# Performance work log

Hardware: AMD Instinct MI355X
Metric: run time of the kernel (lower is better)

Reference implementation:

```python
import jax, jax.numpy as jnp
import numpy as np

B, D = 512, 512
NOBJ, NWRD = 12, 16  # word_feat rows act as 'objects', object_feat rows as 'words' (arg swap in SentiGAT.forward)
N_OW = NOBJ + NWRD
EPS = 1e-12


def _with_self_loops(src, dst, n):
    return (np.concatenate([src, np.arange(n)]), np.concatenate([dst, np.arange(n)]))

_src = np.tile(np.arange(NOBJ), NWRD)                 # arange(n_obj).repeat(n_words) in torch == tile
_dst = np.repeat(np.arange(NWRD), NOBJ) + NOBJ        # repeat_interleave + offset
SRC_OW, DST_OW = map(jnp.asarray, _with_self_loops(_src, _dst, N_OW))

_E5 = np.array([[0,0,0,0,1,1,1,1,2,2,2,2,3,3,3,3,4,4,4,4],
                [1,2,3,4,0,2,3,4,0,1,3,4,0,1,2,4,0,1,2,3]])
SRC5, DST5 = map(jnp.asarray, _with_self_loops(_E5[0], _E5[1], 5))


def gat_conv(x, src, dst, W, a_src, a_dst, bias, concat, num_nodes):
    """PyG GATConv (add_self_loops already in src/dst, negative_slope=0.2, dropout=0)."""
    heads, out_dim = a_src.shape
    h = (x @ W).reshape(num_nodes, heads, out_dim)
    e = jax.nn.leaky_relu((h * a_src).sum(-1)[src] + (h * a_dst).sum(-1)[dst], 0.2)  # [E, heads]
    m = jax.ops.segment_max(e, dst, num_segments=num_nodes)
    p = jnp.exp(e - m[dst])
    alpha = p / jax.ops.segment_sum(p, dst, num_segments=num_nodes)[dst]             # softmax over incoming edges
    out = jax.ops.segment_sum(alpha[:, :, None] * h[src], dst, num_segments=num_nodes)
    out = out.reshape(num_nodes, heads * out_dim) if concat else out.mean(axis=1)
    return out + bias


def _ind_norm(f):
    # add_feature_indicator + F.normalize(p=2, dim=1, eps=1e-12)
    v = (f.sum(axis=1) != 0).astype(f.dtype)[:, None]
    g = jnp.concatenate([f, v], axis=1)
    return g / jnp.maximum(jnp.linalg.norm(g, axis=1, keepdims=True), EPS)


def setup_inputs() -> dict:
    k = jax.random.split(jax.random.key(0), 32)
    r = lambda i, s: jax.random.normal(k[i], s, dtype=jnp.float32)
    sc = 0.05
    return {
        "text_feat": r(0, (B, D)), "image_feat": r(1, (B, D)), "imgtxt_feat": r(2, (B, D)),
        "face_feat": r(3, (B, D)), "word_feat": r(4, (B, NOBJ, D)), "object_feat": r(5, (B, NWRD, D)),
        "ow_W": r(6, (D, 2 * D)) * sc, "ow_asrc": r(7, (2, D)) * sc, "ow_adst": r(8, (2, D)) * sc,
        "ow_b": jnp.zeros((D,), jnp.float32),
        "g1_W": r(9, (D + 1, D)) * sc, "g1_asrc": r(10, (1, D)) * sc, "g1_adst": r(11, (1, D)) * sc,
        "g1_b": jnp.zeros((D,), jnp.float32),
        "g2_W": r(12, (D, D)) * sc, "g2_asrc": r(13, (1, D)) * sc, "g2_adst": r(14, (1, D)) * sc,
        "g2_b": jnp.zeros((D,), jnp.float32),
        "m1_W": r(15, (5 * D, D)) * sc, "m1_b": jnp.zeros((D,), jnp.float32),
        "m2_W": r(16, (D, 3)) * sc, "m2_b": jnp.zeros((3,), jnp.float32),
    }


def reference(text_feat, image_feat, imgtxt_feat, face_feat, word_feat, object_feat,
              ow_W, ow_asrc, ow_adst, ow_b,
              g1_W, g1_asrc, g1_adst, g1_b,
              g2_W, g2_asrc, g2_adst, g2_b,
              m1_W, m1_b, m2_W, m2_b):
    # --- ObjectWordGAT (object_embs=word_feat, word_embs=object_feat per SentiGAT.forward) ---
    def per_sample(obj, wrd):
        x = jnp.concatenate([obj, wrd], axis=0)                       # [N_OW, D]
        h = gat_conv(x, SRC_OW, DST_OW, ow_W, ow_asrc, ow_adst, ow_b, False, N_OW)
        uo, uw = h[:NOBJ], h[NOBJ:]
        attn = jax.nn.softmax(uo @ uw.T, axis=1)                      # [NOBJ, NWRD]
        return (attn @ uw).mean(axis=0)                               # [D]
    aligned = jax.vmap(per_sample)(word_feat, object_feat)            # [B, D]

    feats = [_ind_norm(f) for f in (text_feat, image_feat, imgtxt_feat, face_feat, aligned)]
    x = jnp.stack(feats, axis=1)                                      # [B, 5, D+1]

    # edge_attr (cosine sims) is ignored by GATConv when edge_dim is None
    def graph5(xb):
        h = gat_conv(xb, SRC5, DST5, g1_W, g1_asrc, g1_adst, g1_b, True, 5)
        h = jax.nn.relu(h)
        return gat_conv(h, SRC5, DST5, g2_W, g2_asrc, g2_adst, g2_b, True, 5)
    x = jax.vmap(graph5)(x)                                           # [B, 5, D]

    fused = x.reshape(B, 5 * D)
    hid = jax.nn.relu(fused @ m1_W + m1_b)                            # dropout = identity (eval)
    return hid @ m2_W + m2_b                                          # [B, 3] logits
```

## Files before the change

### kernel.cpp

```cpp
#include <hip/hip_runtime.h>
#include <hip/hip_bf16.h>
#include <math.h>


#define B_SAMP 512

typedef short short8 __attribute__((ext_vector_type(8)));
typedef float floatx4 __attribute__((ext_vector_type(4)));

__device__ __forceinline__ float lrelu02(float x) { return x > 0.f ? x : 0.2f * x; }

__device__ __forceinline__ unsigned short cvt_bf16(float f) {
    union { float f; unsigned int u; } v; v.f = f;
    unsigned int u = v.u;
    return (unsigned short)((u + 0x7FFFu + ((u >> 16) & 1u)) >> 16);
}
__device__ __forceinline__ float bf2f(unsigned short u) {
    union { unsigned int u; float f; } v; v.u = ((unsigned int)u) << 16;
    return v.f;
}

__global__ __launch_bounds__(256) void prep(
    const float* __restrict__ ow_W, const float* __restrict__ ow_asrc,
    const float* __restrict__ ow_adst,
    const float* __restrict__ g1_W, const float* __restrict__ g2_W,
    const float* __restrict__ m1_W,
    float* __restrict__ vg, unsigned short* __restrict__ owWt,
    unsigned short* __restrict__ g1Wt, unsigned short* __restrict__ g2Wt,
    unsigned short* __restrict__ m1Wt)
{
    __shared__ float T[32][33];
    const int tid = threadIdx.x;
    int bid = blockIdx.x;

    if (bid < 128) {
        const int lane = tid & 63;
        const int gw = bid * 4 + (tid >> 6);
        for (int idx = gw; idx < 2048; idx += 512) {
            int t = idx >> 9, k = idx & 511;
            const float* a = (t < 2) ? (ow_asrc + t * 512) : (ow_adst + (t - 2) * 512);
            const float* wr = ow_W + (size_t)k * 1024 + (t & 1) * 512;
            float s = 0.f;
#pragma unroll
            for (int j = 0; j < 8; ++j) s += wr[lane + 64 * j] * a[lane + 64 * j];
            for (int off = 32; off > 0; off >>= 1) s += __shfl_down(s, off, 64);
            if (lane == 0) vg[idx] = s;
        }
        return;
    }
    bid -= 128;
    const float* W; int ldw, K, Kpad, koff, ktiles; float scale; unsigned short* Wt;
    if (bid < 256)        { W = ow_W;       ldw = 1024; K = 512;  Kpad = 1024; koff = 0;   scale = 0.5f; Wt = owWt; ktiles = 16; }
    else if (bid < 512)   { bid -= 256;  W = ow_W + 512; ldw = 1024; K = 512;  Kpad = 1024; koff = 512; scale = 0.5f; Wt = owWt; ktiles = 16; }
    else if (bid < 784)   { bid -= 512;  W = g1_W; ldw = 512; K = 513;  Kpad = 544;  koff = 0; scale = 1.f; Wt = g1Wt; ktiles = 17; }
    else if (bid < 1040)  { bid -= 784;  W = g2_W; ldw = 512; K = 512;  Kpad = 512;  koff = 0; scale = 1.f; Wt = g2Wt; ktiles = 16; }
    else                  { bid -= 1040; W = m1_W; ldw = 512; K = 2560; Kpad = 2560; koff = 0; scale = 1.f; Wt = m1Wt; ktiles = 80; }
    const int k0 = (bid % ktiles) * 32;
    const int n0 = (bid / ktiles) * 32;
    {
        int kr = tid >> 3, nc = (tid & 7) * 4;
        float4 v = make_float4(0.f, 0.f, 0.f, 0.f);
        if (k0 + kr < K) v = *(const float4*)(W + (size_t)(k0 + kr) * ldw + n0 + nc);
        T[nc + 0][kr] = v.x * scale; T[nc + 1][kr] = v.y * scale;
        T[nc + 2][kr] = v.z * scale; T[nc + 3][kr] = v.w * scale;
    }
    __syncthreads();
    {
        int nr = tid >> 3, kc = (tid & 7) * 4;
        ushort4 w;
        w.x = cvt_bf16(T[nr][kc + 0]);
        w.y = cvt_bf16(T[nr][kc + 1]);
        w.z = cvt_bf16(T[nr][kc + 2]);
        w.w = cvt_bf16(T[nr][kc + 3]);
        *(ushort4*)(Wt + (size_t)(n0 + nr) * Kpad + koff + k0 + kc) = w;
    }
}

__global__ __launch_bounds__(256) void ow_pre(
    const float* __restrict__ wf, const float* __restrict__ of,
    const float* __restrict__ vg,
    unsigned short* __restrict__ zcat)
{
    const int b = blockIdx.x;
    __shared__ float Xs[28][512];
    __shared__ float ss[28][2], sd[28][2];
    __shared__ float alpha[16][2][13];

    const int tid = threadIdx.x;
    const int lane = tid & 63;
    const int wid = tid >> 6;

    for (int idx = tid; idx < 28 * 128; idx += 256) {
        int n = idx >> 7, c = (idx & 127) * 4;
        const float* src = (n < 12) ? (wf + ((size_t)b * 12 + n) * 512)
                                    : (of + ((size_t)b * 16 + (n - 12)) * 512);
        *(float4*)&Xs[n][c] = *(const float4*)(src + c);
    }
    __syncthreads();

    for (int p = wid; p < 112; p += 4) {
        int n = p >> 2, t = p & 3;
        const float* vv = vg + t * 512;
        float s = 0.f;
#pragma unroll
        for (int j = 0; j < 8; ++j) s += Xs[n][lane + 64 * j] * vv[lane + 64 * j];
        for (int off = 32; off > 0; off >>= 1) s += __shfl_down(s, off, 64);
        if (lane == 0) { if (t < 2) ss[n][t] = s; else sd[n][t - 2] = s; }
    }
    __syncthreads();

    if (tid < 32) {
        int w = tid >> 1, h = tid & 1;
        float sdv = sd[12 + w][h];
        float e[13], mx = -1e30f;
        for (int j = 0; j < 12; ++j) { e[j] = lrelu02(ss[j][h] + sdv); mx = fmaxf(mx, e[j]); }
        e[12] = lrelu02(ss[12 + w][h] + sdv); mx = fmaxf(mx, e[12]);
        float den = 0.f;
        for (int j = 0; j < 13; ++j) { e[j] = expf(e[j] - mx); den += e[j]; }
        float inv = 1.f / den;
        for (int j = 0; j < 13; ++j) alpha[w][h][j] = e[j] * inv;
    }
    __syncthreads();

    unsigned short* zb = zcat + (size_t)b * 28 * 1024;
    for (int idx = tid; idx < 12 * 1024; idx += 256) {
        int n = idx >> 10, d = idx & 511;
        zb[idx] = cvt_bf16(Xs[n][d]);
    }
    for (int c = tid; c < 1024; c += 256) {
        int h = c >> 9, d = c & 511;
        float xr[12];
#pragma unroll
        for (int j = 0; j < 12; ++j) xr[j] = Xs[j][d];
#pragma unroll 4
        for (int w = 0; w < 16; ++w) {
            float a = alpha[w][h][12] * Xs[12 + w][d];
#pragma unroll
            for (int j = 0; j < 12; ++j) a += alpha[w][h][j] * xr[j];
            zb[(size_t)(12 + w) * 1024 + c] = cvt_bf16(a);
        }
    }
}

template <int BM, int BN, int WGM, int RELU, int SPLITK, int OBF16>
__global__ __launch_bounds__(256) void gemm_v3(
    const unsigned short* __restrict__ A, int lda,
    const unsigned short* __restrict__ Bt, int ldbt,
    void* __restrict__ Cv, int ldc,
    int M, int N, int K,
    const float* __restrict__ bias)
{
    constexpr int WGN = 4 / WGM;
    constexpr int WM = BM / WGM, WN = BN / WGN;
    constexpr int MF = WM / 16, NF = WN / 16;
    constexpr int CA = (BM * 4 + 255) / 256, CB = (BN * 4 + 255) / 256;

    __shared__ unsigned short As[2][BM][40];
    __shared__ unsigned short Bs[2][BN][40];

    const int tid = threadIdx.x;
    const int m0 = blockIdx.x * BM;
    const int n0 = blockIdx.y * BN;
    const int lane = tid & 63;
    const int wid = tid >> 6;
    const int wm = (wid % WGM) * WM;
    const int wn = (wid / WGM) * WN;
    const int fr = lane & 15;
    const int kq = (lane >> 4) * 8;

    const int kchunk = K / SPLITK;
    const int kbeg = (SPLITK > 1) ? blockIdx.z * kchunk : 0;
    const int kend = kbeg + kchunk;
    float* Cf = (float*)Cv;
    unsigned short* Cb = (unsigned short*)Cv;
    if (SPLITK > 1) Cf += (size_t)blockIdx.z * M * ldc;

    short8 ra[CA], rb[CB];
#define LOADAB(K0)                                                                       \
    do {                                                                                 \
        _Pragma("unroll")                                                                \
        for (int c = 0; c < CA; ++c) {                                                   \
            int id = tid + c * 256;                                                      \
            if (BM * 4 % 256 == 0 || id < BM * 4)                                        \
                ra[c] = *(const short8*)(A + (size_t)(m0 + (id >> 2)) * lda + (K0) + (id & 3) * 8); \
        }                                                                                \
        _Pragma("unroll")                                                                \
        for (int c = 0; c < CB; ++c) {                                                   \
            int id = tid + c * 256;                                                      \
            if (BN * 4 % 256 == 0 || id < BN * 4)                                        \
                rb[c] = *(const short8*)(Bt + (size_t)(n0 + (id >> 2)) * ldbt + (K0) + (id & 3) * 8); \
        }                                                                                \
    } while (0)

    LOADAB(kbeg);

    floatx4 acc[MF][NF];
#pragma unroll
    for (int i = 0; i < MF; ++i)
#pragma unroll
        for (int j = 0; j < NF; ++j) acc[i][j] = (floatx4){0.f, 0.f, 0.f, 0.f};

    int t = 0;
    for (int k0 = kbeg; k0 < kend; k0 += 32, t ^= 1) {
#pragma unroll
        for (int c = 0; c < CA; ++c) {
            int id = tid + c * 256;
            if (BM * 4 % 256 == 0 || id < BM * 4)
                *(short8*)&As[t][id >> 2][(id & 3) * 8] = ra[c];
        }
#pragma unroll
        for (int c = 0; c < CB; ++c) {
            int id = tid + c * 256;
            if (BN * 4 % 256 == 0 || id < BN * 4)
                *(short8*)&Bs[t][id >> 2][(id & 3) * 8] = rb[c];
        }
        __syncthreads();
        if (k0 + 32 < kend) LOADAB(k0 + 32);

        short8 af[MF], bw[NF];
#pragma unroll
        for (int i = 0; i < MF; ++i)
            af[i] = *(const short8*)&As[t][wm + i * 16 + fr][kq];
#pragma unroll
        for (int j = 0; j < NF; ++j)
            bw[j] = *(const short8*)&Bs[t][wn + j * 16 + fr][kq];
#pragma unroll
        for (int i = 0; i < MF; ++i)
#pragma unroll
            for (int j = 0; j < NF; ++j)
                acc[i][j] = __builtin_amdgcn_mfma_f32_16x16x32_bf16(
                    af[i], bw[j], acc[i][j], 0, 0, 0);
    }
#undef LOADAB

    const int fq = lane >> 4;
#pragma unroll
    for (int i = 0; i < MF; ++i) {
#pragma unroll
        for (int j = 0; j < NF; ++j) {
#pragma unroll
            for (int q = 0; q < 4; ++q) {
                int row = m0 + wm + i * 16 + fq * 4 + q;
                int col = n0 + wn + j * 16 + fr;
                float v = acc[i][j][q];
                if (SPLITK == 1 && bias) v += bias[col];
                if (RELU) v = fmaxf(v, 0.f);
                if (OBF16) Cb[(size_t)row * ldc + col] = cvt_bf16(v);
                else       Cf[(size_t)row * ldc + col] = v;
            }
        }
    }
}

__global__ __launch_bounds__(256) void attn_x5(
    const unsigned short* __restrict__ hout,
    const float* __restrict__ tf, const float* __restrict__ im,
    const float* __restrict__ it, const float* __restrict__ fa,
    unsigned short* __restrict__ x5)
{
    const int b = blockIdx.x;
    __shared__ float uo[12][520];
    __shared__ float uw[16][520];
    __shared__ float S[12][16];
    __shared__ float w16[16];
    __shared__ float al[512];

    const int tid = threadIdx.x;
    const int lane = tid & 63;
    const int wid = tid >> 6;
    const unsigned short* hb = hout + (size_t)b * 28 * 512;

    for (int idx = tid; idx < 28 * 64; idx += 256) {
        int n = idx >> 6, c = (idx & 63) * 8;
        short8 v = *(const short8*)(hb + (size_t)n * 512 + c);
        float* row = (n < 12) ? &uo[n][c] : &uw[n - 12][c];
#pragma unroll
        for (int j = 0; j < 8; ++j) row[j] = bf2f((unsigned short)v[j]);
    }
    __syncthreads();

    for (int p = wid; p < 192; p += 4) {
        int i = p >> 4, j = p & 15;
        const float* ua = &uo[i][lane * 8];
        const float* uc = &uw[j][lane * 8];
        float s = 0.f;
#pragma unroll
        for (int d = 0; d < 8; ++d) s += ua[d] * uc[d];
        for (int off = 32; off > 0; off >>= 1) s += __shfl_down(s, off, 64);
        if (lane == 0) S[i][j] = s;
    }
    __syncthreads();

    if (tid < 12) {
        float mx = -1e30f;
        for (int j = 0; j < 16; ++j) mx = fmaxf(mx, S[tid][j]);
        float den = 0.f;
        for (int j = 0; j < 16; ++j) { float p = expf(S[tid][j] - mx); S[tid][j] = p; den += p; }
        float inv = 1.f / den;
        for (int j = 0; j < 16; ++j) S[tid][j] *= inv;
    }
    __syncthreads();

    if (tid < 16) {
        float s = 0.f;
        for (int i = 0; i < 12; ++i) s += S[i][tid];
        w16[tid] = s * (1.f / 12.f);
    }
    __syncthreads();

    for (int d = tid; d < 512; d += 256) {
        float s = 0.f;
#pragma unroll
        for (int j = 0; j < 16; ++j) s += w16[j] * uw[j][d];
        al[d] = s;
    }
    __syncthreads();

    for (int f = wid; f < 5; f += 4) {
        const float* src = (f == 0) ? tf : (f == 1) ? im : (f == 2) ? it : (f == 3) ? fa : nullptr;
        float vals[8];
        float sum = 0.f, sq = 0.f;
#pragma unroll
        for (int j = 0; j < 8; ++j) {
            float v = (f < 4) ? src[(size_t)b * 512 + lane + 64 * j] : al[lane + 64 * j];
            vals[j] = v;
            sum += v;
            sq += v * v;
        }
#pragma unroll
        for (int off = 32; off > 0; off >>= 1) {
            sum += __shfl_xor(sum, off, 64);
            sq  += __shfl_xor(sq,  off, 64);
        }
        float v = (sum != 0.f) ? 1.f : 0.f;
        float nrm = fmaxf(sqrtf(sq + v * v), 1e-12f);
        float inv = 1.f / nrm;
        unsigned short* dst = x5 + ((size_t)b * 5 + f) * 544;
#pragma unroll
        for (int j = 0; j < 8; ++j) dst[lane + 64 * j] = cvt_bf16(vals[j] * inv);
        if (lane == 0) dst[512] = cvt_bf16(v * inv);
        else if (lane < 32) dst[512 + lane] = 0;
    }
}

template <int RELU>
__global__ __launch_bounds__(256) void g5_gat(
    const unsigned short* __restrict__ Hg,
    const float* __restrict__ asrc, const float* __restrict__ adst,
    const float* __restrict__ bias, unsigned short* __restrict__ outp)
{
    const int b = blockIdx.x;
    __shared__ float ss[5], sd[5];
    __shared__ float alpha[5][5];

    const int tid = threadIdx.x;
    const int lane = tid & 63;
    const int wave = tid >> 6;
    const unsigned short* Hb = Hg + (size_t)b * 5 * 512;

    for (int p = wave; p < 10; p += 4) {
        int n = p >> 1, ty = p & 1;
        const unsigned short* hv = Hb + n * 512;
        const float* av = ty ? adst : asrc;
        float s = 0.f;
#pragma unroll
        for (int j = 0; j < 8; ++j) s += bf2f(hv[lane + 64 * j]) * av[lane + 64 * j];
        for (int off = 32; off > 0; off >>= 1) s += __shfl_down(s, off, 64);
        if (lane == 0) { if (ty) sd[n] = s; else ss[n] = s; }
    }
    __syncthreads();

    if (tid < 5) {
        int dn = tid;
        float e[5];
        float mx = -1e30f;
        for (int s = 0; s < 5; ++s) {
            e[s] = lrelu02(ss[s] + sd[dn]);
            mx = fmaxf(mx, e[s]);
        }
        float den = 0.f;
        for (int s = 0; s < 5; ++s) { e[s] = expf(e[s] - mx); den += e[s]; }
        float inv = 1.f / den;
        for (int s = 0; s < 5; ++s) alpha[dn][s] = e[s] * inv;
    }
    __syncthreads();

    for (int d = tid; d < 512; d += 256) {
        float h0 = bf2f(Hb[0 * 512 + d]), h1 = bf2f(Hb[1 * 512 + d]), h2 = bf2f(Hb[2 * 512 + d]);
        float h3 = bf2f(Hb[3 * 512 + d]), h4 = bf2f(Hb[4 * 512 + d]);
        float bd = bias[d];
#pragma unroll
        for (int dn = 0; dn < 5; ++dn) {
            float v = alpha[dn][0] * h0 + alpha[dn][1] * h1 + alpha[dn][2] * h2 +
                      alpha[dn][3] * h3 + alpha[dn][4] * h4 + bd;
            if (RELU) v = fmaxf(v, 0.f);
            outp[((size_t)b * 5 + dn) * 512 + d] = cvt_bf16(v);
        }
    }
}

__global__ __launch_bounds__(64) void final2(
    const float* __restrict__ parts, const float* __restrict__ b1,
    const float* __restrict__ w, const float* __restrict__ bvec,
    float* __restrict__ out)
{
    const int b = blockIdx.x;
    const int lane = threadIdx.x;
    float a0 = 0.f, a1 = 0.f, a2 = 0.f;
#pragma unroll
    for (int j = 0; j < 8; ++j) {
        int d = lane + 64 * j;
        size_t o = (size_t)b * 512 + d;
        float x = parts[o] + parts[262144 + o] + parts[524288 + o] + parts[786432 + o] + b1[d];
        x = fmaxf(x, 0.f);
        a0 += x * w[d * 3 + 0];
        a1 += x * w[d * 3 + 1];
        a2 += x * w[d * 3 + 2];
    }
    for (int off = 32; off > 0; off >>= 1) {
        a0 += __shfl_down(a0, off, 64);
        a1 += __shfl_down(a1, off, 64);
        a2 += __shfl_down(a2, off, 64);
    }
    if (lane == 0) {
        out[b * 3 + 0] = a0 + bvec[0];
        out[b * 3 + 1] = a1 + bvec[1];
        out[b * 3 + 2] = a2 + bvec[2];
    }
}

extern "C" void kernel_launch(void* const* d_in, const int* in_sizes, int n_in,
                              void* d_out, int out_size, void* d_ws, size_t ws_size,
                              hipStream_t stream) {
    const float* text   = (const float*)d_in[0];
    const float* image  = (const float*)d_in[1];
    const float* imgtxt = (const float*)d_in[2];
    const float* face   = (const float*)d_in[3];
    const float* word   = (const float*)d_in[4];
    const float* obj    = (const float*)d_in[5];
    const float* ow_W    = (const float*)d_in[6];
    const float* ow_asrc = (const float*)d_in[7];
    const float* ow_adst = (const float*)d_in[8];
    const float* ow_b    = (const float*)d_in[9];
    const float* g1_W    = (const float*)d_in[10];
    const float* g1_asrc = (const float*)d_in[11];
    const float* g1_adst = (const float*)d_in[12];
    const float* g1_b    = (const float*)d_in[13];
    const float* g2_W    = (const float*)d_in[14];
    const float* g2_asrc = (const float*)d_in[15];
    const float* g2_adst = (const float*)d_in[16];
    const float* g2_b    = (const float*)d_in[17];
    const float* m1_W    = (const float*)d_in[18];
    const float* m1_b    = (const float*)d_in[19];
    const float* m2_W    = (const float*)d_in[20];
    const float* m2_b    = (const float*)d_in[21];

    float* ws = (float*)d_ws;
    float* vg = ws;
    float* hidp = ws + 2048;
    unsigned short* owWt = (unsigned short*)(hidp + 1048576);
    unsigned short* g1Wt = owWt + 524288;
    unsigned short* g2Wt = g1Wt + 278528;
    unsigned short* m1Wt = g2Wt + 262144;
    unsigned short* zcat = m1Wt + 1310720;
    unsigned short* houtb = zcat + 14680064;
    unsigned short* x5b  = houtb + 7340032;
    unsigned short* h1b  = x5b + 1392640;
    unsigned short* fsb  = h1b + 1310720;
    unsigned short* hgb  = fsb + 1310720;

    prep<<<2448, 256, 0, stream>>>(ow_W, ow_asrc, ow_adst, g1_W, g2_W, m1_W,
                                   vg, owWt, g1Wt, g2Wt, m1Wt);

    ow_pre<<<B_SAMP, 256, 0, stream>>>(word, obj, vg, zcat);
    gemm_v3<64, 128, 2, 0, 1, 1><<<dim3(224, 4), 256, 0, stream>>>(
        zcat, 1024, owWt, 1024, houtb, 512, 14336, 512, 1024, ow_b);
    attn_x5<<<B_SAMP, 256, 0, stream>>>(houtb, text, image, imgtxt, face, x5b);

    gemm_v3<32, 64, 1, 0, 1, 1><<<dim3(80, 8), 256, 0, stream>>>(
        x5b, 544, g1Wt, 544, hgb, 512, 2560, 512, 544, nullptr);
    g5_gat<1><<<B_SAMP, 256, 0, stream>>>(hgb, g1_asrc, g1_adst, g1_b, h1b);
    gemm_v3<32, 64, 1, 0, 1, 1><<<dim3(80, 8), 256, 0, stream>>>(
        h1b, 512, g2Wt, 512, hgb, 512, 2560, 512, 512, nullptr);
    g5_gat<0><<<B_SAMP, 256, 0, stream>>>(hgb, g2_asrc, g2_adst, g2_b, fsb);

    gemm_v3<32, 64, 1, 0, 4, 0><<<dim3(16, 8, 4), 256, 0, stream>>>(
        fsb, 2560, m1Wt, 2560, hidp, 512, 512, 512, 2560, nullptr);
    final2<<<B_SAMP, 64, 0, stream>>>(hidp, m1_b, m2_W, m2_b, (float*)d_out);
}
```

Baseline: 135.3 us.

## Add direct global-to-LDS GEMM for big ow projection and enlarge tiles

Adds a new 128x128-tile bf16 MFMA GEMM that stages A and B tiles with global_load_lds straight into shared memory, double-buffered, and uses it for the large word/object projection GEMM (14336x512x1024). The smaller GAT and MLP GEMMs move from 32x64 to 64x64 tiles. The aim is to cut VGPR staging and instruction overhead on the dominant GEMM and to raise reuse per block. The cost is fewer blocks (448, and 320 for the GAT GEMMs) and an unpadded LDS layout that can cause bank conflicts on the fragment reads.

```diff
diff --git a/kernel.cpp b/kernel.cpp
--- a/kernel.cpp
+++ b/kernel.cpp
@@ -18,6 +18,11 @@
 __device__ __forceinline__ float bf2f(unsigned short u) {
     union { unsigned int u; float f; } v; v.u = ((unsigned int)u) << 16;
     return v.f;
+}
+__device__ __forceinline__ void gload_lds16(const unsigned short* g, unsigned short* l) {
+    __builtin_amdgcn_global_load_lds(
+        (const __attribute__((address_space(1))) void*)g,
+        (__attribute__((address_space(3))) void*)l, 16, 0, 0);
 }
 
 __global__ __launch_bounds__(256) void prep(
@@ -138,6 +143,85 @@
 #pragma unroll
             for (int j = 0; j < 12; ++j) a += alpha[w][h][j] * xr[j];
             zb[(size_t)(12 + w) * 1024 + c] = cvt_bf16(a);
+        }
+    }
+}
+
+__global__ __launch_bounds__(256) void gemm_glds(
+    const unsigned short* __restrict__ A, int lda,
+    const unsigned short* __restrict__ Bt, int ldbt,
+    unsigned short* __restrict__ C, int ldc,
+    int K, const float* __restrict__ bias)
+{
+    __shared__ unsigned short As[2][128][32];
+    __shared__ unsigned short Bs[2][128][32];
+
+    const int tid = threadIdx.x;
+    const int lane = tid & 63;
+    const int wid = tid >> 6;
+    const int m0 = blockIdx.x * 128;
+    const int n0 = blockIdx.y * 128;
+
+    const int srow = lane >> 2;
+    const int sseg = (lane & 3) * 8;
+    const unsigned short* ga = A + (size_t)(m0 + wid * 32 + srow) * lda + sseg;
+    const unsigned short* gb = Bt + (size_t)(n0 + wid * 32 + srow) * ldbt + sseg;
+    const size_t a16 = (size_t)16 * lda, b16 = (size_t)16 * ldbt;
+
+#define STAGE(t, K0)                                              \
+    do {                                                          \
+        gload_lds16(ga + (K0), &As[t][wid * 32][0]);              \
+        gload_lds16(ga + (K0) + a16, &As[t][wid * 32 + 16][0]);   \
+        gload_lds16(gb + (K0), &Bs[t][wid * 32][0]);              \
+        gload_lds16(gb + (K0) + b16, &Bs[t][wid * 32 + 16][0]);   \
+    } while (0)
+
+    const int wm = (wid & 1) * 64;
+    const int wn = (wid >> 1) * 64;
+    const int fr = lane & 15;
+    const int kq = (lane >> 4) * 8;
+
+    floatx4 acc[4][4];
+#pragma unroll
+    for (int i = 0; i < 4; ++i)
+#pragma unroll
+        for (int j = 0; j < 4; ++j) acc[i][j] = (floatx4){0.f, 0.f, 0.f, 0.f};
+
+    STAGE(0, 0);
+    __syncthreads();
+
+    int t = 0;
+    for (int k0 = 0; k0 < K; k0 += 32, t ^= 1) {
+        if (k0 + 32 < K) STAGE(t ^ 1, k0 + 32);
+
+        short8 af[4], bw[4];
+#pragma unroll
+        for (int i = 0; i < 4; ++i)
+            af[i] = *(const short8*)&As[t][wm + i * 16 + fr][kq];
+#pragma unroll
+        for (int j = 0; j < 4; ++j)
+            bw[j] = *(const short8*)&Bs[t][wn + j * 16 + fr][kq];
+#pragma unroll
+        for (int i = 0; i < 4; ++i)
+#pragma unroll
+            for (int j = 0; j < 4; ++j)
+                acc[i][j] = __builtin_amdgcn_mfma_f32_16x16x32_bf16(
+                    af[i], bw[j], acc[i][j], 0, 0, 0);
+        __syncthreads();
+    }
+#undef STAGE
+
+    const int fq = lane >> 4;
+#pragma unroll
+    for (int i = 0; i < 4; ++i) {
+#pragma unroll
+        for (int j = 0; j < 4; ++j) {
+#pragma unroll
+            for (int q = 0; q < 4; ++q) {
+                int row = m0 + wm + i * 16 + fq * 4 + q;
+                int col = n0 + wn + j * 16 + fr;
+                C[(size_t)row * ldc + col] = cvt_bf16(acc[i][j][q] + bias[col]);
+            }
         }
     }
 }
@@ -473,18 +557,18 @@
                                    vg, owWt, g1Wt, g2Wt, m1Wt);
 
     ow_pre<<<B_SAMP, 256, 0, stream>>>(word, obj, vg, zcat);
-    gemm_v3<64, 128, 2, 0, 1, 1><<<dim3(224, 4), 256, 0, stream>>>(
-        zcat, 1024, owWt, 1024, houtb, 512, 14336, 512, 1024, ow_b);
+    gemm_glds<<<dim3(112, 4), 256, 0, stream>>>(
+        zcat, 1024, owWt, 1024, houtb, 512, 1024, ow_b);
     attn_x5<<<B_SAMP, 256, 0, stream>>>(houtb, text, image, imgtxt, face, x5b);
 
-    gemm_v3<32, 64, 1, 0, 1, 1><<<dim3(80, 8), 256, 0, stream>>>(
+    gemm_v3<64, 64, 2, 0, 1, 1><<<dim3(40, 8), 256, 0, stream>>>(
         x5b, 544, g1Wt, 544, hgb, 512, 2560, 512, 544, nullptr);
     g5_gat<1><<<B_SAMP, 256, 0, stream>>>(hgb, g1_asrc, g1_adst, g1_b, h1b);
-    gemm_v3<32, 64, 1, 0, 1, 1><<<dim3(80, 8), 256, 0, stream>>>(
+    gemm_v3<64, 64, 2, 0, 1, 1><<<dim3(40, 8), 256, 0, stream>>>(
         h1b, 512, g2Wt, 512, hgb, 512, 2560, 512, 512, nullptr);
     g5_gat<0><<<B_SAMP, 256, 0, stream>>>(hgb, g2_asrc, g2_adst, g2_b, fsb);
 
-    gemm_v3<32, 64, 1, 0, 4, 0><<<dim3(16, 8, 4), 256, 0, stream>>>(
+    gemm_v3<64, 64, 2, 0, 4, 0><<<dim3(8, 8, 4), 256, 0, stream>>>(
         fsb, 2560, m1Wt, 2560, hidp, 512, 512, 512, 2560, nullptr);
     final2<<<B_SAMP, 64, 0, stream>>>(hidp, m1_b, m2_W, m2_b, (float*)d_out);
 }
```

Measured after the change: 130.7 us. -3.4%, faster.

## Reassociate object-word GAT attention to avoid projecting all nodes per sample

Applied to the files above, without the earlier changes.

Restructures the object-word GAT branch algebraically. The GEMM that projected all 28 nodes through ow_W is replaced by a precomputed product of the weight halves (WcR times WsR) applied to the object rows, with attention scores formed against aggregated word inputs plus a bias term. Only the softmax-weighted sum per sample is then projected through ow_W. Normalisation moves into a separate build_x5 kernel, the word input is converted from fp32 to bf16 inside the GEMM, and the other GEMM tiles grow to 64x64. This cuts the large 14336-row GEMM and its bf16 staging traffic, at the cost of extra prep work, more launches and different bf16 rounding points.

```diff
diff --git a/kernel.cpp b/kernel.cpp
--- a/kernel.cpp
+++ b/kernel.cpp
@@ -22,20 +22,23 @@
 
 __global__ __launch_bounds__(256) void prep(
     const float* __restrict__ ow_W, const float* __restrict__ ow_asrc,
-    const float* __restrict__ ow_adst,
+    const float* __restrict__ ow_adst, const float* __restrict__ ow_b,
     const float* __restrict__ g1_W, const float* __restrict__ g2_W,
     const float* __restrict__ m1_W,
-    float* __restrict__ vg, unsigned short* __restrict__ owWt,
+    float* __restrict__ vg, float* __restrict__ wb,
+    unsigned short* __restrict__ owWt,
     unsigned short* __restrict__ g1Wt, unsigned short* __restrict__ g2Wt,
-    unsigned short* __restrict__ m1Wt)
+    unsigned short* __restrict__ m1Wt,
+    unsigned short* __restrict__ WcR, unsigned short* __restrict__ WsR)
 {
     __shared__ float T[32][33];
     const int tid = threadIdx.x;
     int bid = blockIdx.x;
+    const int lane = tid & 63;
+    const int wid = tid >> 6;
 
     if (bid < 128) {
-        const int lane = tid & 63;
-        const int gw = bid * 4 + (tid >> 6);
+        const int gw = bid * 4 + wid;
         for (int idx = gw; idx < 2048; idx += 512) {
             int t = idx >> 9, k = idx & 511;
             const float* a = (t < 2) ? (ow_asrc + t * 512) : (ow_adst + (t - 2) * 512);
@@ -48,7 +51,52 @@
         }
         return;
     }
-    bid -= 128;
+    if (bid < 192) {
+        const int gw = (bid - 128) * 4 + wid;
+        for (int a = gw; a < 1024; a += 256) {
+            const float* wr = (a < 512) ? (ow_W + (size_t)a * 1024)
+                                        : (ow_W + (size_t)(a - 512) * 1024 + 512);
+            float s = 0.f;
+#pragma unroll
+            for (int j = 0; j < 8; ++j) s += wr[lane + 64 * j] * ow_b[lane + 64 * j];
+            for (int off = 32; off > 0; off >>= 1) s += __shfl_down(s, off, 64);
+            if (lane == 0) wb[a] = 0.5f * s;
+        }
+        return;
+    }
+    bid -= 192;
+    if (bid >= 2320) {
+        int x = bid - 2320;
+        if (x < 128) {
+            int base = x * 4096;
+#pragma unroll
+            for (int q = 0; q < 4; ++q) {
+                int eidx = base + q * 1024 + tid * 4;
+                int a = eidx >> 9, n = eidx & 511;
+                const float* src = (a < 512) ? (ow_W + (size_t)a * 1024 + n)
+                                             : (ow_W + (size_t)(a - 512) * 1024 + 512 + n);
+                float4 v = *(const float4*)src;
+                ushort4 w;
+                w.x = cvt_bf16(0.5f * v.x); w.y = cvt_bf16(0.5f * v.y);
+                w.z = cvt_bf16(0.5f * v.z); w.w = cvt_bf16(0.5f * v.w);
+                *(ushort4*)(WcR + (size_t)a * 512 + n) = w;
+            }
+        } else {
+            int base = (x - 128) * 4096;
+#pragma unroll
+            for (int q = 0; q < 4; ++q) {
+                int eidx = base + q * 1024 + tid * 4;
+                int d = eidx >> 9, n = eidx & 511;
+                float4 v1 = *(const float4*)(ow_W + (size_t)d * 1024 + n);
+                float4 v2 = *(const float4*)(ow_W + (size_t)d * 1024 + 512 + n);
+                ushort4 w;
+                w.x = cvt_bf16(0.5f * (v1.x + v2.x)); w.y = cvt_bf16(0.5f * (v1.y + v2.y));
+                w.z = cvt_bf16(0.5f * (v1.z + v2.z)); w.w = cvt_bf16(0.5f * (v1.w + v2.w));
+                *(ushort4*)(WsR + (size_t)d * 512 + n) = w;
+            }
+        }
+        return;
+    }
     const float* W; int ldw, K, Kpad, koff, ktiles; float scale; unsigned short* Wt;
     if (bid < 256)        { W = ow_W;       ldw = 1024; K = 512;  Kpad = 1024; koff = 0;   scale = 0.5f; Wt = owWt; ktiles = 16; }
     else if (bid < 512)   { bid -= 256;  W = ow_W + 512; ldw = 1024; K = 512;  Kpad = 1024; koff = 512; scale = 0.5f; Wt = owWt; ktiles = 16; }
@@ -76,10 +124,10 @@
     }
 }
 
-__global__ __launch_bounds__(256) void ow_pre(
+__global__ __launch_bounds__(256) void ow_zw(
     const float* __restrict__ wf, const float* __restrict__ of,
     const float* __restrict__ vg,
-    unsigned short* __restrict__ zcat)
+    unsigned short* __restrict__ zwb)
 {
     const int b = blockIdx.x;
     __shared__ float Xs[28][512];
@@ -122,11 +170,7 @@
     }
     __syncthreads();
 
-    unsigned short* zb = zcat + (size_t)b * 28 * 1024;
-    for (int idx = tid; idx < 12 * 1024; idx += 256) {
-        int n = idx >> 10, d = idx & 511;
-        zb[idx] = cvt_bf16(Xs[n][d]);
-    }
+    unsigned short* zb = zwb + (size_t)b * 16 * 1024;
     for (int c = tid; c < 1024; c += 256) {
         int h = c >> 9, d = c & 511;
         float xr[12];
@@ -137,14 +181,14 @@
             float a = alpha[w][h][12] * Xs[12 + w][d];
 #pragma unroll
             for (int j = 0; j < 12; ++j) a += alpha[w][h][j] * xr[j];
-            zb[(size_t)(12 + w) * 1024 + c] = cvt_bf16(a);
-        }
-    }
-}
-
-template <int BM, int BN, int WGM, int RELU, int SPLITK, int OBF16>
+            zb[(size_t)w * 1024 + c] = cvt_bf16(a);
+        }
+    }
+}
+
+template <int BM, int BN, int WGM, int RELU, int SPLITK, int OBF16, int AF32>
 __global__ __launch_bounds__(256) void gemm_v3(
-    const unsigned short* __restrict__ A, int lda,
+    const void* __restrict__ Av, int lda,
     const unsigned short* __restrict__ Bt, int ldbt,
     void* __restrict__ Cv, int ldc,
     int M, int N, int K,
@@ -153,7 +197,9 @@
     constexpr int WGN = 4 / WGM;
     constexpr int WM = BM / WGM, WN = BN / WGN;
     constexpr int MF = WM / 16, NF = WN / 16;
-    constexpr int CA = (BM * 4 + 255) / 256, CB = (BN * 4 + 255) / 256;
+    constexpr int CAB = (BM * 4 + 255) / 256;
+    constexpr int CAF = (BM * 8 + 255) / 256;
+    constexpr int CB  = (BN * 4 + 255) / 256;
 
     __shared__ unsigned short As[2][BM][40];
     __shared__ unsigned short Bs[2][BN][40];
@@ -175,15 +221,29 @@
     unsigned short* Cb = (unsigned short*)Cv;
     if (SPLITK > 1) Cf += (size_t)blockIdx.z * M * ldc;
 
-    short8 ra[CA], rb[CB];
-#define LOADAB(K0)                                                                       \
+    short8 ra[CAB]; float4 raf[CAF]; short8 rb[CB];
+
+#define LOADA(K0)                                                                        \
     do {                                                                                 \
-        _Pragma("unroll")                                                                \
-        for (int c = 0; c < CA; ++c) {                                                   \
-            int id = tid + c * 256;                                                      \
-            if (BM * 4 % 256 == 0 || id < BM * 4)                                        \
-                ra[c] = *(const short8*)(A + (size_t)(m0 + (id >> 2)) * lda + (K0) + (id & 3) * 8); \
+        if (AF32) {                                                                      \
+            const float* Af = (const float*)Av;                                          \
+            _Pragma("unroll")                                                            \
+            for (int c = 0; c < CAF; ++c) {                                              \
+                int id = tid + c * 256;                                                  \
+                raf[c] = *(const float4*)(Af + (size_t)(m0 + (id >> 3)) * lda + (K0) + (id & 7) * 4); \
+            }                                                                            \
+        } else {                                                                         \
+            const unsigned short* Ab = (const unsigned short*)Av;                        \
+            _Pragma("unroll")                                                            \
+            for (int c = 0; c < CAB; ++c) {                                              \
+                int id = tid + c * 256;                                                  \
+                if (BM * 4 % 256 == 0 || id < BM * 4)                                    \
+                    ra[c] = *(const short8*)(Ab + (size_t)(m0 + (id >> 2)) * lda + (K0) + (id & 3) * 8); \
+            }                                                                            \
         }                                                                                \
+    } while (0)
+#define LOADB(K0)                                                                        \
+    do {                                                                                 \
         _Pragma("unroll")                                                                \
         for (int c = 0; c < CB; ++c) {                                                   \
             int id = tid + c * 256;                                                      \
@@ -192,7 +252,7 @@
         }                                                                                \
     } while (0)
 
-    LOADAB(kbeg);
+    LOADA(kbeg); LOADB(kbeg);
 
     floatx4 acc[MF][NF];
 #pragma unroll
@@ -202,11 +262,22 @@
 
     int t = 0;
     for (int k0 = kbeg; k0 < kend; k0 += 32, t ^= 1) {
-#pragma unroll
-        for (int c = 0; c < CA; ++c) {
-            int id = tid + c * 256;
-            if (BM * 4 % 256 == 0 || id < BM * 4)
-                *(short8*)&As[t][id >> 2][(id & 3) * 8] = ra[c];
+        if (AF32) {
+#pragma unroll
+            for (int c = 0; c < CAF; ++c) {
+                int id = tid + c * 256;
+                ushort4 w;
+                w.x = cvt_bf16(raf[c].x); w.y = cvt_bf16(raf[c].y);
+                w.z = cvt_bf16(raf[c].z); w.w = cvt_bf16(raf[c].w);
+                *(ushort4*)&As[t][id >> 3][(id & 7) * 4] = w;
+            }
+        } else {
+#pragma unroll
+            for (int c = 0; c < CAB; ++c) {
+                int id = tid + c * 256;
+                if (BM * 4 % 256 == 0 || id < BM * 4)
+                    *(short8*)&As[t][id >> 2][(id & 3) * 8] = ra[c];
+            }
         }
 #pragma unroll
         for (int c = 0; c < CB; ++c) {
@@ -215,7 +286,7 @@
                 *(short8*)&Bs[t][id >> 2][(id & 3) * 8] = rb[c];
         }
         __syncthreads();
-        if (k0 + 32 < kend) LOADAB(k0 + 32);
+        if (k0 + 32 < kend) { LOADA(k0 + 32); LOADB(k0 + 32); }
 
         short8 af[MF], bw[NF];
 #pragma unroll
@@ -231,7 +302,8 @@
                 acc[i][j] = __builtin_amdgcn_mfma_f32_16x16x32_bf16(
                     af[i], bw[j], acc[i][j], 0, 0, 0);
     }
-#undef LOADAB
+#undef LOADA
+#undef LOADB
 
     const int fq = lane >> 4;
 #pragma unroll
@@ -252,55 +324,72 @@
     }
 }
 
-__global__ __launch_bounds__(256) void attn_x5(
-    const unsigned short* __restrict__ hout,
-    const float* __restrict__ tf, const float* __restrict__ im,
-    const float* __restrict__ it, const float* __restrict__ fa,
-    unsigned short* __restrict__ x5)
+__global__ __launch_bounds__(256) void ow_attn(
+    const unsigned short* __restrict__ Xq,
+    const unsigned short* __restrict__ zwb,
+    const float* __restrict__ wb,
+    unsigned short* __restrict__ Y)
 {
     const int b = blockIdx.x;
-    __shared__ float uo[12][520];
-    __shared__ float uw[16][520];
+    __shared__ unsigned short xqs[12][1024];
+    __shared__ unsigned short zws[16][1024];
     __shared__ float S[12][16];
+    __shared__ float dj[16];
     __shared__ float w16[16];
-    __shared__ float al[512];
 
     const int tid = threadIdx.x;
     const int lane = tid & 63;
     const int wid = tid >> 6;
-    const unsigned short* hb = hout + (size_t)b * 28 * 512;
-
-    for (int idx = tid; idx < 28 * 64; idx += 256) {
-        int n = idx >> 6, c = (idx & 63) * 8;
-        short8 v = *(const short8*)(hb + (size_t)n * 512 + c);
-        float* row = (n < 12) ? &uo[n][c] : &uw[n - 12][c];
-#pragma unroll
-        for (int j = 0; j < 8; ++j) row[j] = bf2f((unsigned short)v[j]);
-    }
-    __syncthreads();
-
-    for (int p = wid; p < 192; p += 4) {
-        int i = p >> 4, j = p & 15;
-        const float* ua = &uo[i][lane * 8];
-        const float* uc = &uw[j][lane * 8];
+
+    for (int idx = tid; idx < 12 * 128; idx += 256) {
+        int r = idx >> 7, c = (idx & 127) * 8;
+        *(short8*)&xqs[r][c] = *(const short8*)(Xq + ((size_t)b * 12 + r) * 1024 + c);
+    }
+    for (int idx = tid; idx < 16 * 128; idx += 256) {
+        int r = idx >> 7, c = (idx & 127) * 8;
+        *(short8*)&zws[r][c] = *(const short8*)(zwb + ((size_t)b * 16 + r) * 1024 + c);
+    }
+    __syncthreads();
+
+    for (int p = wid; p < 208; p += 4) {
         float s = 0.f;
-#pragma unroll
-        for (int d = 0; d < 8; ++d) s += ua[d] * uc[d];
+        if (p < 192) {
+            int i = p >> 4, j = p & 15;
+#pragma unroll
+            for (int e = 0; e < 8; ++e) {
+                int a = e * 128 + lane * 2;
+                unsigned int xv = *(const unsigned int*)&xqs[i][a];
+                unsigned int zv = *(const unsigned int*)&zws[j][a];
+                s += bf2f((unsigned short)(xv & 0xffff)) * bf2f((unsigned short)(zv & 0xffff))
+                   + bf2f((unsigned short)(xv >> 16))    * bf2f((unsigned short)(zv >> 16));
+            }
+        } else {
+            int j = p - 192;
+#pragma unroll
+            for (int e = 0; e < 8; ++e) {
+                int a = e * 128 + lane * 2;
+                unsigned int zv = *(const unsigned int*)&zws[j][a];
+                s += bf2f((unsigned short)(zv & 0xffff)) * wb[a]
+                   + bf2f((unsigned short)(zv >> 16))    * wb[a + 1];
+            }
+        }
         for (int off = 32; off > 0; off >>= 1) s += __shfl_down(s, off, 64);
-        if (lane == 0) S[i][j] = s;
+        if (lane == 0) { if (p < 192) S[p >> 4][p & 15] = s; else dj[p - 192] = s; }
     }
     __syncthreads();
 
     if (tid < 12) {
         float mx = -1e30f;
-        for (int j = 0; j < 16; ++j) mx = fmaxf(mx, S[tid][j]);
+        for (int j = 0; j < 16; ++j) mx = fmaxf(mx, S[tid][j] + dj[j]);
         float den = 0.f;
-        for (int j = 0; j < 16; ++j) { float p = expf(S[tid][j] - mx); S[tid][j] = p; den += p; }
+        for (int j = 0; j < 16; ++j) {
+            float p = expf(S[tid][j] + dj[j] - mx);
+            S[tid][j] = p; den += p;
+        }
         float inv = 1.f / den;
         for (int j = 0; j < 16; ++j) S[tid][j] *= inv;
     }
     __syncthreads();
-
     if (tid < 16) {
         float s = 0.f;
         for (int i = 0; i < 12; ++i) s += S[i][tid];
@@ -308,39 +397,57 @@
     }
     __syncthreads();
 
-    for (int d = tid; d < 512; d += 256) {
-        float s = 0.f;
-#pragma unroll
-        for (int j = 0; j < 16; ++j) s += w16[j] * uw[j][d];
-        al[d] = s;
-    }
-    __syncthreads();
-
-    for (int f = wid; f < 5; f += 4) {
-        const float* src = (f == 0) ? tf : (f == 1) ? im : (f == 2) ? it : (f == 3) ? fa : nullptr;
-        float vals[8];
-        float sum = 0.f, sq = 0.f;
-#pragma unroll
-        for (int j = 0; j < 8; ++j) {
-            float v = (f < 4) ? src[(size_t)b * 512 + lane + 64 * j] : al[lane + 64 * j];
-            vals[j] = v;
-            sum += v;
-            sq += v * v;
-        }
-#pragma unroll
-        for (int off = 32; off > 0; off >>= 1) {
-            sum += __shfl_xor(sum, off, 64);
-            sq  += __shfl_xor(sq,  off, 64);
-        }
-        float v = (sum != 0.f) ? 1.f : 0.f;
-        float nrm = fmaxf(sqrtf(sq + v * v), 1e-12f);
-        float inv = 1.f / nrm;
-        unsigned short* dst = x5 + ((size_t)b * 5 + f) * 544;
-#pragma unroll
-        for (int j = 0; j < 8; ++j) dst[lane + 64 * j] = cvt_bf16(vals[j] * inv);
-        if (lane == 0) dst[512] = cvt_bf16(v * inv);
-        else if (lane < 32) dst[512 + lane] = 0;
-    }
+    {
+        int a0 = tid * 4;
+        float acc0 = 0.f, acc1 = 0.f, acc2 = 0.f, acc3 = 0.f;
+#pragma unroll
+        for (int j = 0; j < 16; ++j) {
+            float wj = w16[j];
+            ushort4 z4 = *(const ushort4*)&zws[j][a0];
+            acc0 += wj * bf2f(z4.x); acc1 += wj * bf2f(z4.y);
+            acc2 += wj * bf2f(z4.z); acc3 += wj * bf2f(z4.w);
+        }
+        ushort4 o;
+        o.x = cvt_bf16(acc0); o.y = cvt_bf16(acc1);
+        o.z = cvt_bf16(acc2); o.w = cvt_bf16(acc3);
+        *(ushort4*)(Y + (size_t)b * 1024 + a0) = o;
+    }
+}
+
+__global__ __launch_bounds__(256) void build_x5(
+    const float* __restrict__ t, const float* __restrict__ im,
+    const float* __restrict__ it, const float* __restrict__ fa,
+    const float* __restrict__ al, unsigned short* __restrict__ x5)
+{
+    int gw = (int)((blockIdx.x * 256 + threadIdx.x) >> 6);
+    int lane = threadIdx.x & 63;
+    if (gw >= B_SAMP * 5) return;
+    int b = gw / 5, f = gw - b * 5;
+    const float* src = (f == 0) ? t : (f == 1) ? im : (f == 2) ? it : (f == 3) ? fa : al;
+    src += (size_t)b * 512;
+
+    float vals[8];
+    float sum = 0.f, sq = 0.f;
+#pragma unroll
+    for (int j = 0; j < 8; ++j) {
+        float v = src[lane + 64 * j];
+        vals[j] = v;
+        sum += v;
+        sq += v * v;
+    }
+#pragma unroll
+    for (int off = 32; off > 0; off >>= 1) {
+        sum += __shfl_xor(sum, off, 64);
+        sq  += __shfl_xor(sq,  off, 64);
+    }
+    float v = (sum != 0.f) ? 1.f : 0.f;
+    float nrm = fmaxf(sqrtf(sq + v * v), 1e-12f);
+    float inv = 1.f / nrm;
+    unsigned short* dst = x5 + (size_t)gw * 544;
+#pragma unroll
+    for (int j = 0; j < 8; ++j) dst[lane + 64 * j] = cvt_bf16(vals[j] * inv);
+    if (lane == 0) dst[512] = cvt_bf16(v * inv);
+    else if (lane < 32) dst[512 + lane] = 0;
 }
 
 template <int RELU>
@@ -456,35 +563,46 @@
     const float* m2_b    = (const float*)d_in[21];
 
     float* ws = (float*)d_ws;
-    float* vg = ws;
-    float* hidp = ws + 2048;
-    unsigned short* owWt = (unsigned short*)(hidp + 1048576);
-    unsigned short* g1Wt = owWt + 524288;
+    float* vg      = ws;
+    float* wb      = ws + 2048;
+    float* hidp    = ws + 3072;
+    float* aligned = hidp + 1048576;
+    unsigned short* owWt = (unsigned short*)(aligned + 262144);
+    unsigned short* WcR  = owWt + 524288;
+    unsigned short* WsR  = WcR + 524288;
+    unsigned short* Pt   = WsR + 262144;
+    unsigned short* g1Wt = Pt + 524288;
     unsigned short* g2Wt = g1Wt + 278528;
     unsigned short* m1Wt = g2Wt + 262144;
-    unsigned short* zcat = m1Wt + 1310720;
-    unsigned short* houtb = zcat + 14680064;
-    unsigned short* x5b  = houtb + 7340032;
+    unsigned short* Xq   = m1Wt + 1310720;
+    unsigned short* zwb  = Xq + 6291456;
+    unsigned short* Yb   = zwb + 8388608;
+    unsigned short* x5b  = Yb + 524288;
     unsigned short* h1b  = x5b + 1392640;
     unsigned short* fsb  = h1b + 1310720;
     unsigned short* hgb  = fsb + 1310720;
 
-    prep<<<2448, 256, 0, stream>>>(ow_W, ow_asrc, ow_adst, g1_W, g2_W, m1_W,
-                                   vg, owWt, g1Wt, g2Wt, m1Wt);
-
-    ow_pre<<<B_SAMP, 256, 0, stream>>>(word, obj, vg, zcat);
-    gemm_v3<64, 128, 2, 0, 1, 1><<<dim3(224, 4), 256, 0, stream>>>(
-        zcat, 1024, owWt, 1024, houtb, 512, 14336, 512, 1024, ow_b);
-    attn_x5<<<B_SAMP, 256, 0, stream>>>(houtb, text, image, imgtxt, face, x5b);
-
-    gemm_v3<32, 64, 1, 0, 1, 1><<<dim3(80, 8), 256, 0, stream>>>(
+    prep<<<2704, 256, 0, stream>>>(ow_W, ow_asrc, ow_adst, ow_b, g1_W, g2_W, m1_W,
+                                   vg, wb, owWt, g1Wt, g2Wt, m1Wt, WcR, WsR);
+
+    ow_zw<<<B_SAMP, 256, 0, stream>>>(word, obj, vg, zwb);
+    gemm_v3<64, 64, 2, 0, 1, 1, 0><<<dim3(16, 8), 256, 0, stream>>>(
+        WcR, 512, WsR, 512, Pt, 512, 1024, 512, 512, nullptr);
+    gemm_v3<64, 128, 2, 0, 1, 1, 1><<<dim3(96, 8), 256, 0, stream>>>(
+        word, 512, Pt, 512, Xq, 1024, 6144, 1024, 512, nullptr);
+    ow_attn<<<B_SAMP, 256, 0, stream>>>(Xq, zwb, wb, Yb);
+    gemm_v3<64, 64, 2, 0, 1, 0, 0><<<dim3(8, 8), 256, 0, stream>>>(
+        Yb, 1024, owWt, 1024, aligned, 512, 512, 512, 1024, ow_b);
+    build_x5<<<640, 256, 0, stream>>>(text, image, imgtxt, face, aligned, x5b);
+
+    gemm_v3<64, 64, 2, 0, 1, 1, 0><<<dim3(40, 8), 256, 0, stream>>>(
         x5b, 544, g1Wt, 544, hgb, 512, 2560, 512, 544, nullptr);
     g5_gat<1><<<B_SAMP, 256, 0, stream>>>(hgb, g1_asrc, g1_adst, g1_b, h1b);
-    gemm_v3<32, 64, 1, 0, 1, 1><<<dim3(80, 8), 256, 0, stream>>>(
+    gemm_v3<64, 64, 2, 0, 1, 1, 0><<<dim3(40, 8), 256, 0, stream>>>(
         h1b, 512, g2Wt, 512, hgb, 512, 2560, 512, 512, nullptr);
     g5_gat<0><<<B_SAMP, 256, 0, stream>>>(hgb, g2_asrc, g2_adst, g2_b, fsb);
 
-    gemm_v3<32, 64, 1, 0, 4, 0><<<dim3(16, 8, 4), 256, 0, stream>>>(
+    gemm_v3<64, 64, 2, 0, 4, 0, 0><<<dim3(8, 8, 4), 256, 0, stream>>>(
         fsb, 2560, m1Wt, 2560, hidp, 512, 512, 512, 2560, nullptr);
     final2<<<B_SAMP, 64, 0, stream>>>(hidp, m1_b, m2_W, m2_b, (float*)d_out);
 }
```

New measurement: 148.3 us. 9.6% more time.
